# Kernel optimization log

Measured on AMD Instinct MI355X. Metric: run time of the kernel, lower is better.

## Reference

```python
import jax, jax.numpy as jnp
import numpy as np

B, S, D_EMBED, D_HIDDEN = 4, 256, 300, 300
C = 5.0  # frozen tanh-scaling constant


def setup_inputs() -> dict:
    key = jax.random.key(0)
    ks = jax.random.split(key, 8)
    w = 0.05  # ~xavier scale for 300x300
    return {
        "inputs": jax.random.normal(ks[0], (B, S, D_EMBED), jnp.float32),
        "rep_mask": jax.random.randint(ks[1], (B, S), 0, 2, jnp.int32),
        "W_fc": jax.random.normal(ks[2], (D_HIDDEN, D_EMBED), jnp.float32) * w,
        "b_fc": jnp.zeros((D_HIDDEN,), jnp.float32),
        "W1": jax.random.normal(ks[3], (D_HIDDEN, D_HIDDEN), jnp.float32) * w,
        "W2": jax.random.normal(ks[4], (D_HIDDEN, D_HIDDEN), jnp.float32) * w,
        "b1": jnp.zeros((D_HIDDEN,), jnp.float32),
        "W_f1": jax.random.normal(ks[5], (D_HIDDEN, D_HIDDEN), jnp.float32) * w,
        "W_f2": jax.random.normal(ks[6], (D_HIDDEN, D_HIDDEN), jnp.float32) * w,
        "b_f": jnp.zeros((D_HIDDEN,), jnp.float32),
    }


def _disa_fwd(inputs, rep_mask_f, W_fc, b_fc, W1, W2, b1, W_f1, W_f2, b_f):
    n_seq = inputs.shape[1]
    # forward direction mask: attend to strictly later positions (triu, diag=1)
    direct = jnp.triu(jnp.ones((n_seq, n_seq), inputs.dtype), k=1)
    # mask[b,i,j] = rep_mask[b,j] * direct[i,j], shape [B,S,S,1]
    mask = (rep_mask_f[:, None, :] * direct[None]) [..., None]

    rep_map = jax.nn.elu(jnp.einsum('bse,he->bsh', inputs, W_fc) + b_fc)  # [B,S,D]
    dep = jnp.einsum('bsh,gh->bsg', rep_map, W1)   # dependent (token j)
    head = jnp.einsum('bsh,gh->bsg', rep_map, W2)  # head (token i)

    # logits[b,i,j,d]
    logits = C * jnp.tanh((dep[:, None, :, :] + head[:, :, None, :] + b1) / C)

    # hand-rolled masked softmax over dim=2 (j), faithful to original
    masked = logits * mask
    mx = jnp.max(masked, axis=2, keepdims=True)
    exps = jnp.exp(masked - mx) * mask
    sums = jnp.sum(exps, axis=2, keepdims=True)
    sums = sums + (sums == 0).astype(logits.dtype)
    attn = (exps / (sums + 1e-20)) * mask

    attn_result = jnp.sum(attn * rep_map[:, None, :, :], axis=2)  # [B,S,D]

    gate = jax.nn.sigmoid(
        jnp.einsum('bsh,gh->bsg', rep_map, W_f1)
        + jnp.einsum('bsh,gh->bsg', attn_result, W_f2)
        + b_f
    )
    out = gate * rep_map + (1.0 - gate) * attn_result
    return out * rep_mask_f[..., None]


def reference(inputs, rep_mask, W_fc, b_fc, W1, W2, b1, W_f1, W_f2, b_f):
    rep_mask_f = rep_mask.astype(inputs.dtype)
    return _disa_fwd(inputs, rep_mask_f, W_fc, b_fc, W1, W2, b1, W_f1, W_f2, b_f)
```

## Files before the change

### kernel.cpp

```cpp
#include <hip/hip_runtime.h>
#include <hip/hip_bf16.h>

#define Dx 300

#define ED     0
#define HEADF  614400
#define ATTNF  921600
#define U_BASE 1228800
#define REPB   0
#define ATB    327680
#define SYNC_FOFF 2000000

#define AG __HIP_MEMORY_SCOPE_AGENT

typedef __attribute__((ext_vector_type(8))) short short8;
typedef __attribute__((ext_vector_type(4))) float f32x4;

union S8 { unsigned int u[4]; unsigned short s[8]; short8 v; };

__device__ __forceinline__ float bf2f(unsigned short u) {
    union { unsigned int i; float f; } v; v.i = ((unsigned int)u) << 16; return v.f;
}
__device__ __forceinline__ unsigned short f2bf(float x) {
    union { float f; unsigned int i; } u; u.f = x;
    return (unsigned short)((u.i + 0x8000u) >> 16);
}
__device__ __forceinline__ float ldf(const void* p, int idx, int isbf) {
    return isbf ? bf2f(((const unsigned short*)p)[idx]) : ((const float*)p)[idx];
}

__device__ __forceinline__ void st_wt_f32(float* p, float v) {
    asm volatile("global_store_dword %0, %1, off sc0 sc1"
                 :: "v"(p), "v"(v) : "memory");
}
__device__ __forceinline__ void st_wt_u16(unsigned short* p, unsigned short v) {
    unsigned int vv = v;
    asm volatile("global_store_short %0, %1, off sc0 sc1"
                 :: "v"(p), "v"(vv) : "memory");
}

__device__ __forceinline__ void load8f(const float* rowp, int kb, int kmax,
                                       int valid, float* x) {
    if (valid && kb + 8 <= kmax) {
        float4 a = *(const float4*)(rowp + kb);
        float4 b = *(const float4*)(rowp + kb + 4);
        x[0]=a.x; x[1]=a.y; x[2]=a.z; x[3]=a.w;
        x[4]=b.x; x[5]=b.y; x[6]=b.z; x[7]=b.w;
    } else {
        #pragma unroll
        for (int j = 0; j < 8; ++j) {
            int k = kb + j;
            x[j] = (valid && k < kmax) ? rowp[k] : 0.f;
        }
    }
}
__device__ __forceinline__ short8 pack8(const float* x) {
    S8 H;
    #pragma unroll
    for (int p = 0; p < 4; ++p) {
        union { float f; unsigned int i; } a, b;
        a.f = x[2*p]; b.f = x[2*p+1];
        H.u[p] = ((a.i + 0x8000u) >> 16) | ((b.i + 0x8000u) & 0xFFFF0000u);
    }
    return H.v;
}
__device__ __forceinline__ short8 load8bf(const unsigned short* rowp, int kb,
                                          int kmax, int valid) {
    S8 R;
    if (valid && kb + 8 <= kmax) {
        ushort4 a = *(const ushort4*)(rowp + kb);
        ushort4 b = *(const ushort4*)(rowp + kb + 4);
        R.s[0]=a.x; R.s[1]=a.y; R.s[2]=a.z; R.s[3]=a.w;
        R.s[4]=b.x; R.s[5]=b.y; R.s[6]=b.z; R.s[7]=b.w;
    } else {
        #pragma unroll
        for (int j = 0; j < 8; ++j) {
            int k = kb + j;
            R.s[j] = (valid && k < kmax) ? rowp[k] : (unsigned short)0;
        }
    }
    return R.v;
}
__device__ __forceinline__ short8 loadB(const void* W, int row, int kb, int isbf,
                                        int valid) {
    if (isbf) return load8bf((const unsigned short*)W + row * 300, kb, 300, valid);
    float t[8];
    load8f((const float*)W + row * 300, kb, 300, valid, t);
    return pack8(t);
}

__device__ __forceinline__ int xcd_id() {
    int x;
    asm volatile("s_getreg_b32 %0, hwreg(HW_REG_XCC_ID)" : "=s"(x));
    return x & 7;
}
__device__ __forceinline__ void spin_ge(int* p, int target) {
    int t = 0;
    while (__hip_atomic_load(p, __ATOMIC_RELAXED, AG) < target) {
        __builtin_amdgcn_s_sleep(1);
        if (++t > 500000) break;
    }
    asm volatile("" ::: "memory");
}


__global__ __launch_bounds__(320, 4) void k_fused(
        const void* __restrict__ Xv, const int* __restrict__ mask,
        const void* __restrict__ Wfc, const void* __restrict__ bfc,
        const void* __restrict__ W1,  const void* __restrict__ W2,
        const void* __restrict__ b1v, const void* __restrict__ Wf1,
        const void* __restrict__ Wf2, const void* __restrict__ bfv,
        float* __restrict__ ws, void* __restrict__ outv) {
    __shared__ int s_isbf;
    __shared__ unsigned short vlist[256];
    __shared__ int s_cnt, s_tgt;

    const int tid = threadIdx.x;
    const int blk = blockIdx.x;
    if (tid < 64) {
        float v = bf2f(((const unsigned short*)Wfc)[tid]);
        int ok = fabsf(v) < 1.0f;
        unsigned long long bal = __ballot(ok);
        if (tid == 0) s_isbf = (bal == ~0ull) ? 1 : 0;
    }
    __syncthreads();
    const int isbf = s_isbf;
    unsigned short* U = (unsigned short*)(ws + U_BASE);
    int* S = (int*)(ws + SYNC_FOFF);
    const int xid = xcd_id();

    if (blk < 320 && tid < 256) {
        const int w = tid >> 6, l = tid & 63;
        const int mt = blk / 5, nt = blk % 5;
        const int m0 = mt * 16, lm = l & 15, koff = (l >> 4) * 8;
        const int nrow = nt * 64 + w * 16 + lm;
        const int bval = nrow < 300;
        const int ncl = bval ? nrow : 0;
        f32x4 acc = {0.f, 0.f, 0.f, 0.f};
        if (isbf) {
            const unsigned short* Xp = (const unsigned short*)Xv + (m0 + lm) * 300;
            #pragma unroll
            for (int ks = 0; ks < 10; ++ks) {
                short8 a = load8bf(Xp, ks*32 + koff, 300, 1);
                short8 b = loadB(Wfc, ncl, ks*32 + koff, 1, bval);
                acc = __builtin_amdgcn_mfma_f32_16x16x32_bf16(a, b, acc, 0, 0, 0);
            }
        } else {
            const float* Xp = (const float*)Xv + (m0 + lm) * 300;
            #pragma unroll
            for (int ks = 0; ks < 10; ++ks) {
                float t[8]; load8f(Xp, ks*32 + koff, 300, 1, t);
                short8 a = pack8(t);
                short8 b = loadB(Wfc, ncl, ks*32 + koff, 0, bval);
                acc = __builtin_amdgcn_mfma_f32_16x16x32_bf16(a, b, acc, 0, 0, 0);
            }
        }
        if (bval) {
            float bb = ldf(bfc, nrow, isbf);
            #pragma unroll
            for (int r = 0; r < 4; ++r) {
                int mg = m0 + (l >> 4) * 4 + r;
                float v = acc[r] + bb;
                v = v > 0.f ? v : (__expf(v) - 1.f);
                st_wt_f32(ws + ED + (mg * 300 + nrow) * 2 + 1, v);
                st_wt_u16(U + REPB + mg * 320 + nrow, f2bf(v));
            }
        } else {
            #pragma unroll
            for (int r = 0; r < 4; ++r) {
                int mg = m0 + (l >> 4) * 4 + r;
                st_wt_u16(U + REPB + mg * 320 + nrow, 0);
            }
        }
    }
    __syncthreads();
    if (blk < 320 && tid == 0)
        __hip_atomic_fetch_add(S + (blk / 5) * 64, 1, __ATOMIC_RELAXED, AG);

    {
        const int u = blk;
        const int mt = u / 10, nt = u % 10;
        if (tid == 0) spin_ge(S + mt * 64, 5);
        __syncthreads();
        if (tid < 256) {
            const int w = tid >> 6, l = tid & 63;
            const int m0 = mt * 16, lm = l & 15, koff = (l >> 4) * 8;
            const int ng = nt * 64 + w * 16 + lm;
            const int wsel = ng < 320;
            const int wrow = wsel ? ng : ng - 320;
            const int bval = wrow < 300;
            const int ncl = bval ? wrow : 0;
            const void* Wsel = wsel ? W1 : W2;
            const unsigned short* ap = U + REPB + (m0 + lm) * 320 + koff;
            f32x4 acc = {0.f, 0.f, 0.f, 0.f};
            #pragma unroll
            for (int ks = 0; ks < 10; ++ks) {
                short8 a = *(const short8*)(ap + ks * 32);
                short8 b = loadB(Wsel, ncl, ks*32 + koff, isbf, bval);
                acc = __builtin_amdgcn_mfma_f32_16x16x32_bf16(a, b, acc, 0, 0, 0);
            }
            if (ng < 300) {
                float bb = ldf(b1v, ng, isbf);
                #pragma unroll
                for (int r = 0; r < 4; ++r) {
                    int mg = m0 + (l >> 4) * 4 + r;
                    st_wt_f32(ws + ED + (mg * 300 + ng) * 2,
                              __expf(0.4f * (acc[r] + bb)));
                }
            } else if (ng >= 320 && ng < 620) {
                #pragma unroll
                for (int r = 0; r < 4; ++r) {
                    int mg = m0 + (l >> 4) * 4 + r;
                    st_wt_f32(ws + HEADF + mg * 300 + (ng - 320), acc[r]);
                }
            }
        }
        __syncthreads();
        if (tid == 0) {
            const int bb = mt >> 4;
            int old = __hip_atomic_fetch_add(S + (64 + bb) * 64, 1,
                                             __ATOMIC_RELAXED, AG);
            if (old == 159) {
                #pragma unroll
                for (int x = 0; x < 8; ++x)
                    __hip_atomic_store(S + (68 + bb * 8 + x) * 64, 1,
                                       __ATOMIC_RELAXED, AG);
            }
        }
    }

    if (blk >= 320) {
        const int slot = blk - 320;
        const int bat = slot / 80;
        const int tsl = slot - bat * 80;
        const int base = bat * 256;
        if (tid < 64) {
            int basec = 0;
            #pragma unroll
            for (int c = 0; c < 4; ++c) {
                const int j = c * 64 + tid;
                const int mv = mask[base + j] != 0;
                unsigned long long bal = __ballot(mv);
                int pos = basec + __popcll(bal & ((1ull << tid) - 1ull));
                if (mv) vlist[pos] = (unsigned short)j;
                basec += __popcll(bal);
            }
            if (tid == 0) s_cnt = basec;
        }
        if (tid == 0) spin_ge(S + (68 + bat * 8 + xid) * 64, 1);
        __syncthreads();
        const int cnt = s_cnt;
        for (int un = tsl; 2 * un < cnt; un += 80) {
            const int iu = 2 * un;
            const int ia = vlist[iu];
            const int hasB = (iu + 1 < cnt);
            const int ib = hasB ? vlist[iu + 1] : ia;
            const int ga = base + ia, gb = base + ib;
            const int d = tid;
            if (d >= 300) {
                st_wt_u16(U + ATB + ga * 320 + d, 0);
                if (hasB) st_wt_u16(U + ATB + gb * 320 + d, 0);
            } else {
                const float pwa = __expf(0.4f * ws[HEADF + ga * 300 + d]);
                const float pwb = __expf(0.4f * ws[HEADF + gb * 300 + d]);
                const float2* ep2 = ((const float2*)(ws + ED)) + base * Dx + d;
                float sa = 0.f, ra = 0.f, sb = 0.f, rb = 0.f;
                if (hasB) {
                    const int j = ib;
                    float2 v = ep2[j * Dx];
                    float ua = fmaf(v.x, pwa, 1.0f);
                    float ea = __expf(-10.0f * __builtin_amdgcn_rcpf(ua));
                    sa += ea; ra = fmaf(ea, v.y, ra);
                }
                #pragma unroll 16
                for (int t = iu + 2; t < cnt; ++t) {
                    const int j = vlist[t];
                    float2 v = ep2[j * Dx];
                    float ua = fmaf(v.x, pwa, 1.0f);
                    float ub = fmaf(v.x, pwb, 1.0f);
                    float ea = __expf(-10.0f * __builtin_amdgcn_rcpf(ua));
                    float eb = __expf(-10.0f * __builtin_amdgcn_rcpf(ub));
                    sa += ea; ra = fmaf(ea, v.y, ra);
                    sb += eb; rb = fmaf(eb, v.y, rb);
                }
                const float dena = sa + (sa == 0.f ? 1.f : 0.f) + 1e-20f;
                const float aa = ra / dena;
                st_wt_f32(ws + ATTNF + ga * Dx + d, aa);
                st_wt_u16(U + ATB + ga * 320 + d, f2bf(aa));
                if (hasB) {
                    const float denb = sb + (sb == 0.f ? 1.f : 0.f) + 1e-20f;
                    const float ab = rb / denb;
                    st_wt_f32(ws + ATTNF + gb * Dx + d, ab);
                    st_wt_u16(U + ATB + gb * 320 + d, f2bf(ab));
                }
            }
            __syncthreads();
            if (tid == 0) {
                __hip_atomic_fetch_add(S + (100 + (ga >> 4)) * 64, 1,
                                       __ATOMIC_RELAXED, AG);
                if (hasB)
                    __hip_atomic_fetch_add(S + (100 + (gb >> 4)) * 64, 1,
                                           __ATOMIC_RELAXED, AG);
            }
        }
    }

    if (blk < 320) {
        const int mt3 = blk / 5, nt3 = blk % 5;
        const int m0 = mt3 * 16;
        if (tid < 64) {
            int mv = (tid < 16) ? (mask[m0 + tid] != 0) : 0;
            unsigned long long bal = __ballot(mv);
            if (tid == 0) s_tgt = (int)__popcll(bal);
        }
        __syncthreads();
        const int tgt = s_tgt;
        if (tid == 0 && tgt > 0) spin_ge(S + (100 + mt3) * 64, tgt);
        __syncthreads();
        if (tid < 256) {
            const int w = tid >> 6, l = tid & 63;
            const int lm = l & 15, koff = (l >> 4) * 8;
            const int nrow = nt3 * 64 + w * 16 + lm;
            const int bval = nrow < 300;
            const int ncl = bval ? nrow : 0;
            const unsigned short* a1p = U + REPB + (m0 + lm) * 320 + koff;
            const unsigned short* a2p = U + ATB  + (m0 + lm) * 320 + koff;
            f32x4 acc = {0.f, 0.f, 0.f, 0.f};
            #pragma unroll
            for (int ks = 0; ks < 10; ++ks) {
                short8 a = *(const short8*)(a1p + ks * 32);
                short8 bB = loadB(Wf1, ncl, ks*32 + koff, isbf, bval);
                acc = __builtin_amdgcn_mfma_f32_16x16x32_bf16(a, bB, acc, 0, 0, 0);
            }
            #pragma unroll
            for (int ks = 0; ks < 10; ++ks) {
                short8 a = *(const short8*)(a2p + ks * 32);
                short8 bB = loadB(Wf2, ncl, ks*32 + koff, isbf, bval);
                acc = __builtin_amdgcn_mfma_f32_16x16x32_bf16(a, bB, acc, 0, 0, 0);
            }
            if (bval) {
                float bb = ldf(bfv, nrow, isbf);
                #pragma unroll
                for (int r = 0; r < 4; ++r) {
                    int mg = m0 + (l >> 4) * 4 + r;
                    float res = 0.f;
                    if (mask[mg]) {
                        float gp = acc[r] + bb;
                        float gate = 1.0f / (1.0f + __expf(-gp));
                        float rv = ws[ED + (mg * 300 + nrow) * 2 + 1];
                        float av = ws[ATTNF + mg * 300 + nrow];
                        res = gate * rv + (1.0f - gate) * av;
                    }
                    if (isbf) ((__hip_bfloat16*)outv)[mg * 300 + nrow] = __float2bfloat16(res);
                    else      ((float*)outv)[mg * 300 + nrow] = res;
                }
            }
        }
    }
}

extern "C" void kernel_launch(void* const* d_in, const int* in_sizes, int n_in,
                              void* d_out, int out_size, void* d_ws, size_t ws_size,
                              hipStream_t stream) {
    const void* X   = d_in[0];
    const int*  msk = (const int*)d_in[1];
    const void* Wfc = d_in[2];
    const void* bfc = d_in[3];
    const void* W1  = d_in[4];
    const void* W2  = d_in[5];
    const void* b1  = d_in[6];
    const void* Wf1 = d_in[7];
    const void* Wf2 = d_in[8];
    const void* bfv = d_in[9];
    float* ws = (float*)d_ws;

    hipMemsetAsync((char*)d_ws + (size_t)SYNC_FOFF * sizeof(float), 0, 49152, stream);

    hipLaunchKernelGGL(k_fused, dim3(640), dim3(320), 0, stream,
                       X, msk, Wfc, bfc, W1, W2, b1, Wf1, Wf2, bfv, ws, d_out);
}
```

Before: 121.9 us.

## Partition work per XCD with atomic work-queue and XCD-local workspace

Restructures the fused kernel so each XCD owns one half of one batch, with its own workspace region and sync counters. Blocks pull work units from a per-XCD atomic counter in dependency order (fc GEMM, W1/W2 GEMM, attention rows, gate GEMM), replacing the fixed block-to-stage mapping. Write-through cache-bypassing stores are replaced by plain stores, relying on intra-XCD L2 coherence. The intent is to keep producer/consumer traffic in one XCD's L2 and cut cross-XCD sync latency. The cost is redundant fc and W1/W2 GEMM work across the two halves of each batch. Correctness depends on the XCD id mapping and the grid size being balanced across XCDs.

```diff
diff --git a/kernel.cpp b/kernel.cpp
--- a/kernel.cpp
+++ b/kernel.cpp
@@ -3,15 +3,21 @@
 
 #define Dx 300
 
-#define ED     0
-#define HEADF  614400
-#define ATTNF  921600
-#define U_BASE 1228800
-#define REPB   0
-#define ATB    327680
-#define SYNC_FOFF 2000000
+#define GSTRIDE 331776
+#define EDg     0
+#define HDg     153600
+#define ATg     230400
+#define UOFFg   268800
+#define REPBg   0
+#define ATBg    81920
+#define SYNC_FOFF 2800000
 
 #define AG __HIP_MEMORY_SCOPE_AGENT
+
+#define U_MM2 80
+#define U_ATT 240
+#define U_MM3 304
+#define U_TOT 344
 
 typedef __attribute__((ext_vector_type(8))) short short8;
 typedef __attribute__((ext_vector_type(4))) float f32x4;
@@ -27,16 +33,6 @@
 }
 __device__ __forceinline__ float ldf(const void* p, int idx, int isbf) {
     return isbf ? bf2f(((const unsigned short*)p)[idx]) : ((const float*)p)[idx];
-}
-
-__device__ __forceinline__ void st_wt_f32(float* p, float v) {
-    asm volatile("global_store_dword %0, %1, off sc0 sc1"
-                 :: "v"(p), "v"(v) : "memory");
-}
-__device__ __forceinline__ void st_wt_u16(unsigned short* p, unsigned short v) {
-    unsigned int vv = v;
-    asm volatile("global_store_short %0, %1, off sc0 sc1"
-                 :: "v"(p), "v"(vv) : "memory");
 }
 
 __device__ __forceinline__ void load8f(const float* rowp, int kb, int kmax,
@@ -111,248 +107,251 @@
         const void* __restrict__ b1v, const void* __restrict__ Wf1,
         const void* __restrict__ Wf2, const void* __restrict__ bfv,
         float* __restrict__ ws, void* __restrict__ outv) {
-    __shared__ int s_isbf;
+    __shared__ int s_isbf, s_u, s_cnt, s_c128;
+    __shared__ int s_tgt3[8];
     __shared__ unsigned short vlist[256];
-    __shared__ int s_cnt, s_tgt;
 
     const int tid = threadIdx.x;
-    const int blk = blockIdx.x;
     if (tid < 64) {
         float v = bf2f(((const unsigned short*)Wfc)[tid]);
         int ok = fabsf(v) < 1.0f;
         unsigned long long bal = __ballot(ok);
         if (tid == 0) s_isbf = (bal == ~0ull) ? 1 : 0;
     }
+    if (tid >= 64 && tid < 72) s_tgt3[tid - 64] = 0;
     __syncthreads();
     const int isbf = s_isbf;
-    unsigned short* U = (unsigned short*)(ws + U_BASE);
-    int* S = (int*)(ws + SYNC_FOFF);
-    const int xid = xcd_id();
-
-    if (blk < 320 && tid < 256) {
-        const int w = tid >> 6, l = tid & 63;
-        const int mt = blk / 5, nt = blk % 5;
-        const int m0 = mt * 16, lm = l & 15, koff = (l >> 4) * 8;
-        const int nrow = nt * 64 + w * 16 + lm;
-        const int bval = nrow < 300;
-        const int ncl = bval ? nrow : 0;
-        f32x4 acc = {0.f, 0.f, 0.f, 0.f};
-        if (isbf) {
-            const unsigned short* Xp = (const unsigned short*)Xv + (m0 + lm) * 300;
-            #pragma unroll
-            for (int ks = 0; ks < 10; ++ks) {
-                short8 a = load8bf(Xp, ks*32 + koff, 300, 1);
-                short8 b = loadB(Wfc, ncl, ks*32 + koff, 1, bval);
-                acc = __builtin_amdgcn_mfma_f32_16x16x32_bf16(a, b, acc, 0, 0, 0);
-            }
-        } else {
-            const float* Xp = (const float*)Xv + (m0 + lm) * 300;
-            #pragma unroll
-            for (int ks = 0; ks < 10; ++ks) {
-                float t[8]; load8f(Xp, ks*32 + koff, 300, 1, t);
-                short8 a = pack8(t);
-                short8 b = loadB(Wfc, ncl, ks*32 + koff, 0, bval);
-                acc = __builtin_amdgcn_mfma_f32_16x16x32_bf16(a, b, acc, 0, 0, 0);
-            }
+
+    const int g = xcd_id();
+    const int b = g >> 1, h = g & 1;
+    const int base = b * 256, rbase = base + h * 128;
+    float* G = ws + (size_t)g * GSTRIDE;
+    unsigned short* U = (unsigned short*)(G + UOFFg);
+    int* S = (int*)(ws + SYNC_FOFF) + g * 1024;
+
+    if (tid < 64) {
+        int basec = 0;
+        #pragma unroll
+        for (int c = 0; c < 4; ++c) {
+            const int j = c * 64 + tid;
+            const int mv = mask[base + j] != 0;
+            unsigned long long bal = __ballot(mv);
+            int pos = basec + __popcll(bal & ((1ull << tid) - 1ull));
+            if (mv) vlist[pos] = (unsigned short)j;
+            basec += __popcll(bal);
+            if (c == 1 && tid == 0) s_c128 = basec;
         }
-        if (bval) {
-            float bb = ldf(bfc, nrow, isbf);
-            #pragma unroll
-            for (int r = 0; r < 4; ++r) {
-                int mg = m0 + (l >> 4) * 4 + r;
-                float v = acc[r] + bb;
-                v = v > 0.f ? v : (__expf(v) - 1.f);
-                st_wt_f32(ws + ED + (mg * 300 + nrow) * 2 + 1, v);
-                st_wt_u16(U + REPB + mg * 320 + nrow, f2bf(v));
-            }
-        } else {
-            #pragma unroll
-            for (int r = 0; r < 4; ++r) {
-                int mg = m0 + (l >> 4) * 4 + r;
-                st_wt_u16(U + REPB + mg * 320 + nrow, 0);
-            }
-        }
+        if (tid == 0) s_cnt = basec;
     }
     __syncthreads();
-    if (blk < 320 && tid == 0)
-        __hip_atomic_fetch_add(S + (blk / 5) * 64, 1, __ATOMIC_RELAXED, AG);
-
-    {
-        const int u = blk;
-        const int mt = u / 10, nt = u % 10;
-        if (tid == 0) spin_ge(S + mt * 64, 5);
+    const int cnt = s_cnt;
+    const int lo = h ? s_c128 : 0;
+    const int hi = h ? cnt : s_c128;
+    if (tid < 128) {
+        const int k = lo + tid;
+        if (k < hi) atomicAdd(&s_tgt3[((int)vlist[k] - h * 128) >> 4], 1);
+    }
+    __syncthreads();
+
+    for (;;) {
         __syncthreads();
-        if (tid < 256) {
-            const int w = tid >> 6, l = tid & 63;
-            const int m0 = mt * 16, lm = l & 15, koff = (l >> 4) * 8;
-            const int ng = nt * 64 + w * 16 + lm;
-            const int wsel = ng < 320;
-            const int wrow = wsel ? ng : ng - 320;
-            const int bval = wrow < 300;
-            const int ncl = bval ? wrow : 0;
-            const void* Wsel = wsel ? W1 : W2;
-            const unsigned short* ap = U + REPB + (m0 + lm) * 320 + koff;
-            f32x4 acc = {0.f, 0.f, 0.f, 0.f};
-            #pragma unroll
-            for (int ks = 0; ks < 10; ++ks) {
-                short8 a = *(const short8*)(ap + ks * 32);
-                short8 b = loadB(Wsel, ncl, ks*32 + koff, isbf, bval);
-                acc = __builtin_amdgcn_mfma_f32_16x16x32_bf16(a, b, acc, 0, 0, 0);
-            }
-            if (ng < 300) {
-                float bb = ldf(b1v, ng, isbf);
-                #pragma unroll
-                for (int r = 0; r < 4; ++r) {
-                    int mg = m0 + (l >> 4) * 4 + r;
-                    st_wt_f32(ws + ED + (mg * 300 + ng) * 2,
-                              __expf(0.4f * (acc[r] + bb)));
-                }
-            } else if (ng >= 320 && ng < 620) {
-                #pragma unroll
-                for (int r = 0; r < 4; ++r) {
-                    int mg = m0 + (l >> 4) * 4 + r;
-                    st_wt_f32(ws + HEADF + mg * 300 + (ng - 320), acc[r]);
-                }
-            }
-        }
+        if (tid == 0)
+            s_u = __hip_atomic_fetch_add(S, 1, __ATOMIC_RELAXED, AG);
         __syncthreads();
-        if (tid == 0) {
-            const int bb = mt >> 4;
-            int old = __hip_atomic_fetch_add(S + (64 + bb) * 64, 1,
-                                             __ATOMIC_RELAXED, AG);
-            if (old == 159) {
-                #pragma unroll
-                for (int x = 0; x < 8; ++x)
-                    __hip_atomic_store(S + (68 + bb * 8 + x) * 64, 1,
-                                       __ATOMIC_RELAXED, AG);
-            }
-        }
-    }
-
-    if (blk >= 320) {
-        const int slot = blk - 320;
-        const int bat = slot / 80;
-        const int tsl = slot - bat * 80;
-        const int base = bat * 256;
-        if (tid < 64) {
-            int basec = 0;
-            #pragma unroll
-            for (int c = 0; c < 4; ++c) {
-                const int j = c * 64 + tid;
-                const int mv = mask[base + j] != 0;
-                unsigned long long bal = __ballot(mv);
-                int pos = basec + __popcll(bal & ((1ull << tid) - 1ull));
-                if (mv) vlist[pos] = (unsigned short)j;
-                basec += __popcll(bal);
-            }
-            if (tid == 0) s_cnt = basec;
-        }
-        if (tid == 0) spin_ge(S + (68 + bat * 8 + xid) * 64, 1);
-        __syncthreads();
-        const int cnt = s_cnt;
-        for (int un = tsl; 2 * un < cnt; un += 80) {
-            const int iu = 2 * un;
-            const int ia = vlist[iu];
-            const int hasB = (iu + 1 < cnt);
-            const int ib = hasB ? vlist[iu + 1] : ia;
-            const int ga = base + ia, gb = base + ib;
-            const int d = tid;
-            if (d >= 300) {
-                st_wt_u16(U + ATB + ga * 320 + d, 0);
-                if (hasB) st_wt_u16(U + ATB + gb * 320 + d, 0);
-            } else {
-                const float pwa = __expf(0.4f * ws[HEADF + ga * 300 + d]);
-                const float pwb = __expf(0.4f * ws[HEADF + gb * 300 + d]);
-                const float2* ep2 = ((const float2*)(ws + ED)) + base * Dx + d;
-                float sa = 0.f, ra = 0.f, sb = 0.f, rb = 0.f;
-                if (hasB) {
-                    const int j = ib;
-                    float2 v = ep2[j * Dx];
-                    float ua = fmaf(v.x, pwa, 1.0f);
-                    float ea = __expf(-10.0f * __builtin_amdgcn_rcpf(ua));
-                    sa += ea; ra = fmaf(ea, v.y, ra);
-                }
-                #pragma unroll 16
-                for (int t = iu + 2; t < cnt; ++t) {
-                    const int j = vlist[t];
-                    float2 v = ep2[j * Dx];
-                    float ua = fmaf(v.x, pwa, 1.0f);
-                    float ub = fmaf(v.x, pwb, 1.0f);
-                    float ea = __expf(-10.0f * __builtin_amdgcn_rcpf(ua));
-                    float eb = __expf(-10.0f * __builtin_amdgcn_rcpf(ub));
-                    sa += ea; ra = fmaf(ea, v.y, ra);
-                    sb += eb; rb = fmaf(eb, v.y, rb);
-                }
-                const float dena = sa + (sa == 0.f ? 1.f : 0.f) + 1e-20f;
-                const float aa = ra / dena;
-                st_wt_f32(ws + ATTNF + ga * Dx + d, aa);
-                st_wt_u16(U + ATB + ga * 320 + d, f2bf(aa));
-                if (hasB) {
-                    const float denb = sb + (sb == 0.f ? 1.f : 0.f) + 1e-20f;
-                    const float ab = rb / denb;
-                    st_wt_f32(ws + ATTNF + gb * Dx + d, ab);
-                    st_wt_u16(U + ATB + gb * 320 + d, f2bf(ab));
+        const int u = s_u;
+        if (u >= U_TOT) break;
+
+        if (u < U_MM2) {
+            const int mt = u / 5, nt = u % 5;
+            if (tid < 256) {
+                const int w = tid >> 6, l = tid & 63;
+                const int lm = l & 15, koff = (l >> 4) * 8;
+                const int nrow = nt * 64 + w * 16 + lm;
+                const int bval = nrow < 300;
+                const int ncl = bval ? nrow : 0;
+                f32x4 acc = {0.f, 0.f, 0.f, 0.f};
+                const int arow = base + mt * 16 + lm;
+                if (isbf) {
+                    const unsigned short* Xp = (const unsigned short*)Xv + arow * 300;
+                    #pragma unroll
+                    for (int ks = 0; ks < 10; ++ks) {
+                        short8 a = load8bf(Xp, ks*32 + koff, 300, 1);
+                        short8 bb = loadB(Wfc, ncl, ks*32 + koff, 1, bval);
+                        acc = __builtin_amdgcn_mfma_f32_16x16x32_bf16(a, bb, acc, 0, 0, 0);
+                    }
+                } else {
+                    const float* Xp = (const float*)Xv + arow * 300;
+                    #pragma unroll
+                    for (int ks = 0; ks < 10; ++ks) {
+                        float t[8]; load8f(Xp, ks*32 + koff, 300, 1, t);
+                        short8 a = pack8(t);
+                        short8 bb = loadB(Wfc, ncl, ks*32 + koff, 0, bval);
+                        acc = __builtin_amdgcn_mfma_f32_16x16x32_bf16(a, bb, acc, 0, 0, 0);
+                    }
+                }
+                if (bval) {
+                    float bb = ldf(bfc, nrow, isbf);
+                    #pragma unroll
+                    for (int r = 0; r < 4; ++r) {
+                        const int lr = mt * 16 + (l >> 4) * 4 + r;
+                        float v = acc[r] + bb;
+                        v = v > 0.f ? v : (__expf(v) - 1.f);
+                        G[EDg + (lr * 300 + nrow) * 2 + 1] = v;
+                        U[REPBg + lr * 320 + nrow] = f2bf(v);
+                    }
+                } else {
+                    #pragma unroll
+                    for (int r = 0; r < 4; ++r) {
+                        const int lr = mt * 16 + (l >> 4) * 4 + r;
+                        U[REPBg + lr * 320 + nrow] = 0;
+                    }
                 }
             }
             __syncthreads();
-            if (tid == 0) {
-                __hip_atomic_fetch_add(S + (100 + (ga >> 4)) * 64, 1,
-                                       __ATOMIC_RELAXED, AG);
-                if (hasB)
-                    __hip_atomic_fetch_add(S + (100 + (gb >> 4)) * 64, 1,
+            if (tid == 0)
+                __hip_atomic_fetch_add(S + 32 + mt * 32, 1, __ATOMIC_RELAXED, AG);
+
+        } else if (u < U_ATT) {
+            const int q = u - U_MM2, mt = q / 10, nt10 = q % 10;
+            if (tid == 0) spin_ge(S + 32 + mt * 32, 5);
+            __syncthreads();
+            if (tid < 256) {
+                const int w = tid >> 6, l = tid & 63;
+                const int lm = l & 15, koff = (l >> 4) * 8;
+                const int ng = nt10 * 64 + w * 16 + lm;
+                const int wsel = ng < 320;
+                const int wrow = wsel ? ng : ng - 320;
+                const int bval = wrow < 300;
+                const int ncl = bval ? wrow : 0;
+                const void* Wsel = wsel ? W1 : W2;
+                const unsigned short* ap = U + REPBg + (mt * 16 + lm) * 320 + koff;
+                f32x4 acc = {0.f, 0.f, 0.f, 0.f};
+                #pragma unroll
+                for (int ks = 0; ks < 10; ++ks) {
+                    short8 a = *(const short8*)(ap + ks * 32);
+                    short8 bb = loadB(Wsel, ncl, ks*32 + koff, isbf, bval);
+                    acc = __builtin_amdgcn_mfma_f32_16x16x32_bf16(a, bb, acc, 0, 0, 0);
+                }
+                if (ng < 300) {
+                    float bb = ldf(b1v, ng, isbf);
+                    #pragma unroll
+                    for (int r = 0; r < 4; ++r) {
+                        const int lr = mt * 16 + (l >> 4) * 4 + r;
+                        G[EDg + (lr * 300 + ng) * 2] = __expf(0.4f * (acc[r] + bb));
+                    }
+                } else if (ng >= 320 && ng < 620) {
+                    #pragma unroll
+                    for (int r = 0; r < 4; ++r) {
+                        const int lr = mt * 16 + (l >> 4) * 4 + r;
+                        G[HDg + lr * 300 + (ng - 320)] = acc[r];
+                    }
+                }
+            }
+            __syncthreads();
+            if (tid == 0)
+                __hip_atomic_fetch_add(S + 576, 1, __ATOMIC_RELAXED, AG);
+
+        } else if (u < U_MM3) {
+            const int p = u - U_ATT;
+            const int iu = lo + 2 * p;
+            if (iu < hi) {
+                if (tid == 0) spin_ge(S + 576, 160);
+                __syncthreads();
+                const int ia = vlist[iu];
+                const int hasB = (iu + 1 < hi);
+                const int ib = hasB ? vlist[iu + 1] : ia;
+                const int ha = ia - h * 128, hb = ib - h * 128;
+                const int d = tid;
+                if (d >= 300) {
+                    U[ATBg + ha * 320 + d] = 0;
+                    U[ATBg + hb * 320 + d] = 0;
+                } else {
+                    const float pwa = __expf(0.4f * G[HDg + ia * 300 + d]);
+                    const float pwb = __expf(0.4f * G[HDg + ib * 300 + d]);
+                    const float2* ep2 = ((const float2*)(G + EDg)) + d;
+                    float sa = 0.f, ra = 0.f, sb = 0.f, rb = 0.f;
+                    if (iu + 1 < cnt) {
+                        const int j = vlist[iu + 1];
+                        float2 v = ep2[j * 300];
+                        float ua = fmaf(v.x, pwa, 1.0f);
+                        float ea = __expf(-10.0f * __builtin_amdgcn_rcpf(ua));
+                        sa += ea; ra = fmaf(ea, v.y, ra);
+                    }
+                    #pragma unroll 16
+                    for (int t = iu + 2; t < cnt; ++t) {
+                        const int j = vlist[t];
+                        float2 v = ep2[j * 300];
+                        float ua = fmaf(v.x, pwa, 1.0f);
+                        float ub = fmaf(v.x, pwb, 1.0f);
+                        float ea = __expf(-10.0f * __builtin_amdgcn_rcpf(ua));
+                        float eb = __expf(-10.0f * __builtin_amdgcn_rcpf(ub));
+                        sa += ea; ra = fmaf(ea, v.y, ra);
+                        sb += eb; rb = fmaf(eb, v.y, rb);
+                    }
+                    const float dena = sa + (sa == 0.f ? 1.f : 0.f) + 1e-20f;
+                    const float aa = ra / dena;
+                    G[ATg + ha * 300 + d] = aa;
+                    U[ATBg + ha * 320 + d] = f2bf(aa);
+                    if (hasB) {
+                        const float denb = sb + (sb == 0.f ? 1.f : 0.f) + 1e-20f;
+                        const float ab = rb / denb;
+                        G[ATg + hb * 300 + d] = ab;
+                        U[ATBg + hb * 320 + d] = f2bf(ab);
+                    }
+                }
+                __syncthreads();
+                if (tid == 0) {
+                    __hip_atomic_fetch_add(S + 640 + (ha >> 4) * 32, 1,
                                            __ATOMIC_RELAXED, AG);
+                    if (hasB)
+                        __hip_atomic_fetch_add(S + 640 + (hb >> 4) * 32, 1,
+                                               __ATOMIC_RELAXED, AG);
+                }
             }
-        }
-    }
-
-    if (blk < 320) {
-        const int mt3 = blk / 5, nt3 = blk % 5;
-        const int m0 = mt3 * 16;
-        if (tid < 64) {
-            int mv = (tid < 16) ? (mask[m0 + tid] != 0) : 0;
-            unsigned long long bal = __ballot(mv);
-            if (tid == 0) s_tgt = (int)__popcll(bal);
-        }
-        __syncthreads();
-        const int tgt = s_tgt;
-        if (tid == 0 && tgt > 0) spin_ge(S + (100 + mt3) * 64, tgt);
-        __syncthreads();
-        if (tid < 256) {
-            const int w = tid >> 6, l = tid & 63;
-            const int lm = l & 15, koff = (l >> 4) * 8;
-            const int nrow = nt3 * 64 + w * 16 + lm;
-            const int bval = nrow < 300;
-            const int ncl = bval ? nrow : 0;
-            const unsigned short* a1p = U + REPB + (m0 + lm) * 320 + koff;
-            const unsigned short* a2p = U + ATB  + (m0 + lm) * 320 + koff;
-            f32x4 acc = {0.f, 0.f, 0.f, 0.f};
-            #pragma unroll
-            for (int ks = 0; ks < 10; ++ks) {
-                short8 a = *(const short8*)(a1p + ks * 32);
-                short8 bB = loadB(Wf1, ncl, ks*32 + koff, isbf, bval);
-                acc = __builtin_amdgcn_mfma_f32_16x16x32_bf16(a, bB, acc, 0, 0, 0);
-            }
-            #pragma unroll
-            for (int ks = 0; ks < 10; ++ks) {
-                short8 a = *(const short8*)(a2p + ks * 32);
-                short8 bB = loadB(Wf2, ncl, ks*32 + koff, isbf, bval);
-                acc = __builtin_amdgcn_mfma_f32_16x16x32_bf16(a, bB, acc, 0, 0, 0);
-            }
-            if (bval) {
-                float bb = ldf(bfv, nrow, isbf);
+
+        } else {
+            const int m = u - U_MM3, mt3 = m / 5, nt3 = m % 5;
+            const int tgt = s_tgt3[mt3];
+            if (tid == 0 && tgt > 0) spin_ge(S + 640 + mt3 * 32, tgt);
+            __syncthreads();
+            if (tid < 256) {
+                const int w = tid >> 6, l = tid & 63;
+                const int lm = l & 15, koff = (l >> 4) * 8;
+                const int nrow = nt3 * 64 + w * 16 + lm;
+                const int bval = nrow < 300;
+                const int ncl = bval ? nrow : 0;
+                const unsigned short* a1p = U + REPBg + (h * 128 + mt3 * 16 + lm) * 320 + koff;
+                const unsigned short* a2p = U + ATBg + (mt3 * 16 + lm) * 320 + koff;
+                f32x4 acc = {0.f, 0.f, 0.f, 0.f};
                 #pragma unroll
-                for (int r = 0; r < 4; ++r) {
-                    int mg = m0 + (l >> 4) * 4 + r;
-                    float res = 0.f;
-                    if (mask[mg]) {
-                        float gp = acc[r] + bb;
-                        float gate = 1.0f / (1.0f + __expf(-gp));
-                        float rv = ws[ED + (mg * 300 + nrow) * 2 + 1];
-                        float av = ws[ATTNF + mg * 300 + nrow];
-                        res = gate * rv + (1.0f - gate) * av;
-                    }
-                    if (isbf) ((__hip_bfloat16*)outv)[mg * 300 + nrow] = __float2bfloat16(res);
-                    else      ((float*)outv)[mg * 300 + nrow] = res;
+                for (int ks = 0; ks < 10; ++ks) {
+                    short8 a = *(const short8*)(a1p + ks * 32);
+                    short8 bb = loadB(Wf1, ncl, ks*32 + koff, isbf, bval);
+                    acc = __builtin_amdgcn_mfma_f32_16x16x32_bf16(a, bb, acc, 0, 0, 0);
+                }
+                #pragma unroll
+                for (int ks = 0; ks < 10; ++ks) {
+                    short8 a = *(const short8*)(a2p + ks * 32);
+                    short8 bb = loadB(Wf2, ncl, ks*32 + koff, isbf, bval);
+                    acc = __builtin_amdgcn_mfma_f32_16x16x32_bf16(a, bb, acc, 0, 0, 0);
+                }
+                if (bval) {
+                    float bb = ldf(bfv, nrow, isbf);
+                    #pragma unroll
+                    for (int r = 0; r < 4; ++r) {
+                        const int mgl = mt3 * 16 + (l >> 4) * 4 + r;
+                        const int gr = rbase + mgl;
+                        float res = 0.f;
+                        if (mask[gr]) {
+                            float gp = acc[r] + bb;
+                            float gate = 1.0f / (1.0f + __expf(-gp));
+                            float rv = G[EDg + ((h * 128 + mgl) * 300 + nrow) * 2 + 1];
+                            float av = G[ATg + mgl * 300 + nrow];
+                            res = gate * rv + (1.0f - gate) * av;
+                        }
+                        if (isbf) ((__hip_bfloat16*)outv)[gr * 300 + nrow] = __float2bfloat16(res);
+                        else      ((float*)outv)[gr * 300 + nrow] = res;
+                    }
                 }
             }
         }
@@ -374,8 +373,8 @@
     const void* bfv = d_in[9];
     float* ws = (float*)d_ws;
 
-    hipMemsetAsync((char*)d_ws + (size_t)SYNC_FOFF * sizeof(float), 0, 49152, stream);
-
-    hipLaunchKernelGGL(k_fused, dim3(640), dim3(320), 0, stream,
+    hipMemsetAsync((char*)d_ws + (size_t)SYNC_FOFF * sizeof(float), 0, 32768, stream);
+
+    hipLaunchKernelGGL(k_fused, dim3(768), dim3(320), 0, stream,
                        X, msk, Wfc, bfc, W1, W2, b1, Wf1, Wf2, bfv, ws, d_out);
 }
```

After: 155.3 us. +27.4%, slower.

## Remap blocks so each batch's work is colocated on paired XCDs

Applied to the files above, without the earlier changes.

Replaces the linear block-to-work mapping with one derived from blk&7: each block is assigned to a batch according to its XCD slot pair, and handles GEMM tiles, projection tiles and attention rows for that batch. Previously GEMM blocks (0-319) and attention blocks (320+) were disjoint sets. Now every block runs all phases for its batch, and producer and consumer data stay within the same XCD L2. This adds more serial phases per block and relies on the launch grid size matching the new mapping, with each block handling at most one attention row pair.

```diff
diff --git a/kernel.cpp b/kernel.cpp
--- a/kernel.cpp
+++ b/kernel.cpp
@@ -129,9 +129,15 @@
     int* S = (int*)(ws + SYNC_FOFF);
     const int xid = xcd_id();
 
-    if (blk < 320 && tid < 256) {
+    const int res = blk & 7;
+    const int bat = res >> 1;
+    const int li  = ((blk >> 3) << 1) | (res & 1);
+    const int base = bat * 256;
+
+    if (li < 80 && tid < 256) {
+        const int mt_l = li / 5, nt = li % 5;
+        const int mt = bat * 16 + mt_l;
         const int w = tid >> 6, l = tid & 63;
-        const int mt = blk / 5, nt = blk % 5;
         const int m0 = mt * 16, lm = l & 15, koff = (l >> 4) * 8;
         const int nrow = nt * 64 + w * 16 + lm;
         const int bval = nrow < 300;
@@ -174,18 +180,19 @@
         }
     }
     __syncthreads();
-    if (blk < 320 && tid == 0)
-        __hip_atomic_fetch_add(S + (blk / 5) * 64, 1, __ATOMIC_RELAXED, AG);
+    if (li < 80 && tid == 0)
+        __hip_atomic_fetch_add(S + (bat * 16 + li / 5) * 64, 1,
+                               __ATOMIC_RELAXED, AG);
 
     {
-        const int u = blk;
-        const int mt = u / 10, nt = u % 10;
+        const int mt_l = li / 10, nt10 = li % 10;
+        const int mt = bat * 16 + mt_l;
         if (tid == 0) spin_ge(S + mt * 64, 5);
         __syncthreads();
         if (tid < 256) {
             const int w = tid >> 6, l = tid & 63;
             const int m0 = mt * 16, lm = l & 15, koff = (l >> 4) * 8;
-            const int ng = nt * 64 + w * 16 + lm;
+            const int ng = nt10 * 64 + w * 16 + lm;
             const int wsel = ng < 320;
             const int wrow = wsel ? ng : ng - 320;
             const int bval = wrow < 300;
@@ -217,23 +224,18 @@
         }
         __syncthreads();
         if (tid == 0) {
-            const int bb = mt >> 4;
-            int old = __hip_atomic_fetch_add(S + (64 + bb) * 64, 1,
+            int old = __hip_atomic_fetch_add(S + (64 + bat) * 64, 1,
                                              __ATOMIC_RELAXED, AG);
             if (old == 159) {
                 #pragma unroll
                 for (int x = 0; x < 8; ++x)
-                    __hip_atomic_store(S + (68 + bb * 8 + x) * 64, 1,
+                    __hip_atomic_store(S + (68 + bat * 8 + x) * 64, 1,
                                        __ATOMIC_RELAXED, AG);
             }
         }
     }
 
-    if (blk >= 320) {
-        const int slot = blk - 320;
-        const int bat = slot / 80;
-        const int tsl = slot - bat * 80;
-        const int base = bat * 256;
+    {
         if (tid < 64) {
             int basec = 0;
             #pragma unroll
@@ -250,8 +252,8 @@
         if (tid == 0) spin_ge(S + (68 + bat * 8 + xid) * 64, 1);
         __syncthreads();
         const int cnt = s_cnt;
-        for (int un = tsl; 2 * un < cnt; un += 80) {
-            const int iu = 2 * un;
+        const int iu = 2 * li;
+        if (iu < cnt) {
             const int ia = vlist[iu];
             const int hasB = (iu + 1 < cnt);
             const int ib = hasB ? vlist[iu + 1] : ia;
@@ -305,8 +307,8 @@
         }
     }
 
-    if (blk < 320) {
-        const int mt3 = blk / 5, nt3 = blk % 5;
+    if (li < 80) {
+        const int mt3 = bat * 16 + li / 5, nt3 = li % 5;
         const int m0 = mt3 * 16;
         if (tid < 64) {
             int mv = (tid < 16) ? (mask[m0 + tid] != 0) : 0;
@@ -343,16 +345,16 @@
                 #pragma unroll
                 for (int r = 0; r < 4; ++r) {
                     int mg = m0 + (l >> 4) * 4 + r;
-                    float res = 0.f;
+                    float res2 = 0.f;
                     if (mask[mg]) {
                         float gp = acc[r] + bb;
                         float gate = 1.0f / (1.0f + __expf(-gp));
                         float rv = ws[ED + (mg * 300 + nrow) * 2 + 1];
                         float av = ws[ATTNF + mg * 300 + nrow];
-                        res = gate * rv + (1.0f - gate) * av;
+                        res2 = gate * rv + (1.0f - gate) * av;
                     }
-                    if (isbf) ((__hip_bfloat16*)outv)[mg * 300 + nrow] = __float2bfloat16(res);
-                    else      ((float*)outv)[mg * 300 + nrow] = res;
+                    if (isbf) ((__hip_bfloat16*)outv)[mg * 300 + nrow] = __float2bfloat16(res2);
+                    else      ((float*)outv)[mg * 300 + nrow] = res2;
                 }
             }
         }
```

Result: faster. 114.2 us (-6.3%).
